# Kernel optimization log

Measured on AMD Instinct MI355X. Metric: run time of the kernel, lower is better.

Reference implementation:

```python
import jax, jax.numpy as jnp
import numpy as np

K_LIST = (1, 5, 20)
IGNORE = -100


def setup_inputs() -> dict:
    key = jax.random.key(0)
    k1, k2 = jax.random.split(key)
    logits = jax.random.normal(k1, (2, 2048, 32000), dtype=jnp.float32)
    labels = jax.random.randint(k2, (2, 2048), 0, 32000, dtype=jnp.int64)
    return {"logits": logits, "labels": labels}


def reference(logits, labels):
    B, S, V = logits.shape
    # shift labels left by one, pad with ignore_index (-100)
    extra = jnp.full((B, 1), IGNORE, dtype=labels.dtype)
    shift_labels = jnp.concatenate([labels[:, 1:], extra], axis=1).reshape(-1)  # [B*S]
    lg = logits.reshape(-1, V)  # [N, V]

    valid = shift_labels >= 0
    safe = jnp.where(valid, shift_labels, 0)
    n_valid = valid.sum().astype(lg.dtype)

    # cross entropy per token (Fast_CrossEntropyLoss equivalent)
    lp = jax.nn.log_softmax(lg, axis=-1)  # [N, V]
    ce = -jnp.take_along_axis(lp, safe[:, None], axis=-1)[:, 0]  # [N]
    ce = jnp.where(valid, ce, 0.0)
    loss = ce.sum() / n_valid  # focal_loss_gamma == 0 -> plain mean over valid

    # categorical entropy per token: -sum p * log p
    entropy = -jnp.sum(jnp.exp(lp) * lp, axis=-1)  # [N]
    entropy = jnp.where(valid, entropy, 0.0)

    # top-k accuracies (k = 1, 5, 20) over valid tokens
    _, topk = jax.lax.top_k(lg, max(K_LIST))  # [N, 20]
    hits = topk == safe[:, None]  # [N, 20]
    accs = tuple(
        (jnp.any(hits[:, :k], axis=-1) & valid).sum().astype(lg.dtype) / n_valid
        for k in K_LIST
    )

    # Note: per-token ce/entropy are returned full-length with zeros at
    # invalid positions (jit-compatible masking instead of boolean gather).
    return (loss, ce, entropy, *accs)
```

## Files before the change

### kernel.cpp

```cpp
#include <hip/hip_runtime.h>
#include <math.h>

#define VOCAB 32000
#define NV4   (VOCAB / 4)
#define BLK   256
#define SEQ   2048
#define IGNORE_IDX (-100)

__device__ inline void merge_state(float& m, float& s, float& t,
                                   float om, float os, float ot) {
    float mm = fmaxf(m, om);
    float ca = __expf(m - mm);
    float cb = __expf(om - mm);
    t = ca * (t + (m - mm) * s) + cb * (ot + (om - mm) * os);
    s = ca * s + cb * os;
    m = mm;
}

__global__ void init_ws_kernel(float* ws) {
    if (threadIdx.x < 8) ws[threadIdx.x] = 0.0f;
}

__global__ __launch_bounds__(BLK)
void ce_metrics_kernel(const float* __restrict__ logits,
                       const int* __restrict__ labels,
                       float* __restrict__ out,
                       float* __restrict__ ws,
                       int N)
{
    const int n = blockIdx.x;
    const int pos = n % SEQ;

    float* ce_out  = out + 1;
    float* ent_out = out + 1 + N;

    int label = (pos < SEQ - 1) ? labels[n + 1] : IGNORE_IDX;

    if (label < 0) {
        if (threadIdx.x == 0) { ce_out[n] = 0.0f; ent_out[n] = 0.0f; }
        return;
    }

    const float* __restrict__ row = logits + (size_t)n * VOCAB;
    const float x_label = row[label];
    const float4* __restrict__ row4 = (const float4*)row;

    float m = -3.402823466e38f;
    float s = 0.0f, t = 0.0f;
    int cgt = 0;
    int ceq = 0;

    for (int i = threadIdx.x; i < NV4; i += BLK) {
        float4 x4 = row4[i];
        const float xs[4] = {x4.x, x4.y, x4.z, x4.w};
        #pragma unroll
        for (int j = 0; j < 4; ++j) {
            float x = xs[j];
            if (x > m) {
                float c = __expf(m - x);
                t = c * (t + (m - x) * s);
                s = c * s + 1.0f;
                m = x;
            } else {
                float d = x - m;
                float e = __expf(d);
                s += e;
                t += e * d;
            }
            cgt += (x > x_label) ? 1 : 0;
            ceq += (x == x_label && (4 * i + j) < label) ? 1 : 0;
        }
    }

    #pragma unroll
    for (int mask = 32; mask > 0; mask >>= 1) {
        float om = __shfl_xor(m, mask);
        float os = __shfl_xor(s, mask);
        float ot = __shfl_xor(t, mask);
        cgt += __shfl_xor(cgt, mask);
        ceq += __shfl_xor(ceq, mask);
        merge_state(m, s, t, om, os, ot);
    }

    __shared__ float sm[4], ss[4], st[4];
    __shared__ int sgt[4], seq_[4];
    const int wid  = threadIdx.x >> 6;
    const int lane = threadIdx.x & 63;
    if (lane == 0) { sm[wid] = m; ss[wid] = s; st[wid] = t; sgt[wid] = cgt; seq_[wid] = ceq; }
    __syncthreads();

    if (threadIdx.x == 0) {
        m = sm[0]; s = ss[0]; t = st[0]; cgt = sgt[0]; ceq = seq_[0];
        #pragma unroll
        for (int w = 1; w < 4; ++w) {
            merge_state(m, s, t, sm[w], ss[w], st[w]);
            cgt += sgt[w];
            ceq += seq_[w];
        }
        float logs = logf(s);
        float ce   = m + logs - x_label;
        float ent  = logs - t / s;
        ce_out[n]  = ce;
        ent_out[n] = ent;

        int rank = cgt + ceq;
        atomicAdd(&ws[0], ce);
        atomicAdd(&ws[1], 1.0f);
        if (rank < 1)  atomicAdd(&ws[2], 1.0f);
        if (rank < 5)  atomicAdd(&ws[3], 1.0f);
        if (rank < 20) atomicAdd(&ws[4], 1.0f);
    }
}

__global__ void finalize_kernel(const float* __restrict__ ws,
                                float* __restrict__ out, int N) {
    if (threadIdx.x == 0) {
        float nv = ws[1];
        out[0]         = ws[0] / nv;
        out[1 + 2 * N]     = ws[2] / nv;
        out[1 + 2 * N + 1] = ws[3] / nv;
        out[1 + 2 * N + 2] = ws[4] / nv;
    }
}

extern "C" void kernel_launch(void* const* d_in, const int* in_sizes, int n_in,
                              void* d_out, int out_size, void* d_ws, size_t ws_size,
                              hipStream_t stream) {
    const float* logits = (const float*)d_in[0];
    const int*   labels = (const int*)d_in[1];
    float* out = (float*)d_out;
    float* ws  = (float*)d_ws;

    const int N = in_sizes[1];

    init_ws_kernel<<<1, 64, 0, stream>>>(ws);
    ce_metrics_kernel<<<N, BLK, 0, stream>>>(logits, labels, out, ws, N);
    finalize_kernel<<<1, 64, 0, stream>>>(ws, out, N);
}
```

Before: 716.5 us.

## Map one wavefront per token, vectorize online softmax, replace atomics with two-pass reduction

Each token row is now handled by one 64-lane wavefront instead of a 256-thread block, which removes the shared-memory and __syncthreads cross-wave merge. The per-element branchy online softmax becomes a branch-free update done once per float4, using the max of four elements and a fixed, unrolled trip count. Global atomics and the init kernel are replaced by a per-token rank written to the workspace and a single-block finalize reduction. In exchange each wave streams a 128KB row alone, so more memory parallelism has to come from occupancy across waves, and the finalize pass adds a serial single-block sweep over N entries.

```diff
diff --git a/kernel.cpp b/kernel.cpp
--- a/kernel.cpp
+++ b/kernel.cpp
@@ -3,77 +3,82 @@
 
 #define VOCAB 32000
 #define NV4   (VOCAB / 4)
-#define BLK   256
 #define SEQ   2048
+#define ITERS (NV4 / 64)
 #define IGNORE_IDX (-100)
 
 __device__ inline void merge_state(float& m, float& s, float& t,
                                    float om, float os, float ot) {
     float mm = fmaxf(m, om);
-    float ca = __expf(m - mm);
-    float cb = __expf(om - mm);
-    t = ca * (t + (m - mm) * s) + cb * (ot + (om - mm) * os);
+    float da = fmaxf(m - mm, -64.0f);
+    float db = fmaxf(om - mm, -64.0f);
+    float ca = __expf(da);
+    float cb = __expf(db);
+    t = ca * (t + da * s) + cb * (ot + db * os);
     s = ca * s + cb * os;
     m = mm;
 }
 
-__global__ void init_ws_kernel(float* ws) {
-    if (threadIdx.x < 8) ws[threadIdx.x] = 0.0f;
-}
-
-__global__ __launch_bounds__(BLK)
+__global__ __launch_bounds__(256)
 void ce_metrics_kernel(const float* __restrict__ logits,
                        const int* __restrict__ labels,
                        float* __restrict__ out,
                        float* __restrict__ ws,
                        int N)
 {
-    const int n = blockIdx.x;
-    const int pos = n % SEQ;
+    const int token = (blockIdx.x << 2) + (threadIdx.x >> 6);
+    const int lane  = threadIdx.x & 63;
+    if (token >= N) return;
 
     float* ce_out  = out + 1;
     float* ent_out = out + 1 + N;
 
-    int label = (pos < SEQ - 1) ? labels[n + 1] : IGNORE_IDX;
+    const int pos = token & (SEQ - 1);
+    const int label = (pos < SEQ - 1) ? labels[token + 1] : IGNORE_IDX;
 
     if (label < 0) {
-        if (threadIdx.x == 0) { ce_out[n] = 0.0f; ent_out[n] = 0.0f; }
+        if (lane == 0) { ce_out[token] = 0.0f; ent_out[token] = 0.0f; ws[token] = -1.0f; }
         return;
     }
 
-    const float* __restrict__ row = logits + (size_t)n * VOCAB;
-    const float x_label = row[label];
+    const float* __restrict__ row = logits + (size_t)token * VOCAB;
+    const float xl = row[label];
     const float4* __restrict__ row4 = (const float4*)row;
 
-    float m = -3.402823466e38f;
-    float s = 0.0f, t = 0.0f;
+    float m = -3.402823466e38f, s = 0.0f, t = 0.0f;
     int cgt = 0;
     int ceq = 0;
 
-    for (int i = threadIdx.x; i < NV4; i += BLK) {
-        float4 x4 = row4[i];
-        const float xs[4] = {x4.x, x4.y, x4.z, x4.w};
-        #pragma unroll
-        for (int j = 0; j < 4; ++j) {
-            float x = xs[j];
-            if (x > m) {
-                float c = __expf(m - x);
-                t = c * (t + (m - x) * s);
-                s = c * s + 1.0f;
-                m = x;
-            } else {
-                float d = x - m;
-                float e = __expf(d);
-                s += e;
-                t += e * d;
-            }
-            cgt += (x > x_label) ? 1 : 0;
-            ceq += (x == x_label && (4 * i + j) < label) ? 1 : 0;
-        }
+    #pragma unroll 5
+    for (int it = 0; it < ITERS; ++it) {
+        const int i4 = it * 64 + lane;
+        float4 x4 = row4[i4];
+
+        float m4 = fmaxf(fmaxf(x4.x, x4.y), fmaxf(x4.z, x4.w));
+        float nm = fmaxf(m, m4);
+        float d1 = fmaxf(m - nm, -64.0f);
+        float c  = __expf(d1);
+        float cs = c * s;
+        t = fmaf(d1, cs, c * t);
+        s = cs;
+        m = nm;
+
+        float dx = x4.x - m, dy = x4.y - m, dz = x4.z - m, dw = x4.w - m;
+        float ex = __expf(dx), ey = __expf(dy), ez = __expf(dz), ew = __expf(dw);
+        s += (ex + ey) + (ez + ew);
+        t = fmaf(ex, dx, t); t = fmaf(ey, dy, t);
+        t = fmaf(ez, dz, t); t = fmaf(ew, dw, t);
+
+        const int base = i4 << 2;
+        cgt += (x4.x > xl) + (x4.y > xl) + (x4.z > xl) + (x4.w > xl);
+        ceq += ((x4.x == xl) & (base     < label))
+             + ((x4.y == xl) & (base + 1 < label))
+             + ((x4.z == xl) & (base + 2 < label))
+             + ((x4.w == xl) & (base + 3 < label));
     }
 
     #pragma unroll
-    for (int mask = 32; mask > 0; mask >>= 1) {
+    for (int mask = 32; mask; mask >>= 1) {
         float om = __shfl_xor(m, mask);
         float os = __shfl_xor(s, mask);
         float ot = __shfl_xor(t, mask);
@@ -82,44 +87,55 @@
         merge_state(m, s, t, om, os, ot);
     }
 
-    __shared__ float sm[4], ss[4], st[4];
-    __shared__ int sgt[4], seq_[4];
-    const int wid  = threadIdx.x >> 6;
-    const int lane = threadIdx.x & 63;
-    if (lane == 0) { sm[wid] = m; ss[wid] = s; st[wid] = t; sgt[wid] = cgt; seq_[wid] = ceq; }
-    __syncthreads();
-
-    if (threadIdx.x == 0) {
-        m = sm[0]; s = ss[0]; t = st[0]; cgt = sgt[0]; ceq = seq_[0];
-        #pragma unroll
-        for (int w = 1; w < 4; ++w) {
-            merge_state(m, s, t, sm[w], ss[w], st[w]);
-            cgt += sgt[w];
-            ceq += seq_[w];
-        }
+    if (lane == 0) {
         float logs = logf(s);
-        float ce   = m + logs - x_label;
-        float ent  = logs - t / s;
-        ce_out[n]  = ce;
-        ent_out[n] = ent;
-
-        int rank = cgt + ceq;
-        atomicAdd(&ws[0], ce);
-        atomicAdd(&ws[1], 1.0f);
-        if (rank < 1)  atomicAdd(&ws[2], 1.0f);
-        if (rank < 5)  atomicAdd(&ws[3], 1.0f);
-        if (rank < 20) atomicAdd(&ws[4], 1.0f);
+        ce_out[token]  = m + logs - xl;
+        ent_out[token] = logs - t / s;
+        ws[token] = (float)(cgt + ceq);
     }
 }
 
-__global__ void finalize_kernel(const float* __restrict__ ws,
-                                float* __restrict__ out, int N) {
+__global__ __launch_bounds__(256)
+void finalize_kernel(const float* __restrict__ ws,
+                     float* __restrict__ out, int N)
+{
+    const float* ce = out + 1;
+    float ce_sum = 0.f, nv = 0.f, h1 = 0.f, h5 = 0.f, h20 = 0.f;
+    for (int i = threadIdx.x; i < N; i += 256) {
+        float r = ws[i];
+        if (r >= 0.f) {
+            nv     += 1.f;
+            ce_sum += ce[i];
+            h1  += (r < 1.f)  ? 1.f : 0.f;
+            h5  += (r < 5.f)  ? 1.f : 0.f;
+            h20 += (r < 20.f) ? 1.f : 0.f;
+        }
+    }
+    #pragma unroll
+    for (int mask = 32; mask; mask >>= 1) {
+        ce_sum += __shfl_xor(ce_sum, mask);
+        nv     += __shfl_xor(nv, mask);
+        h1     += __shfl_xor(h1, mask);
+        h5     += __shfl_xor(h5, mask);
+        h20    += __shfl_xor(h20, mask);
+    }
+    __shared__ float red[5][4];
+    const int wid = threadIdx.x >> 6, lane = threadIdx.x & 63;
+    if (lane == 0) {
+        red[0][wid] = ce_sum; red[1][wid] = nv;
+        red[2][wid] = h1; red[3][wid] = h5; red[4][wid] = h20;
+    }
+    __syncthreads();
     if (threadIdx.x == 0) {
-        float nv = ws[1];
-        out[0]         = ws[0] / nv;
-        out[1 + 2 * N]     = ws[2] / nv;
-        out[1 + 2 * N + 1] = ws[3] / nv;
-        out[1 + 2 * N + 2] = ws[4] / nv;
+        ce_sum = red[0][0] + red[0][1] + red[0][2] + red[0][3];
+        nv     = red[1][0] + red[1][1] + red[1][2] + red[1][3];
+        h1     = red[2][0] + red[2][1] + red[2][2] + red[2][3];
+        h5     = red[3][0] + red[3][1] + red[3][2] + red[3][3];
+        h20    = red[4][0] + red[4][1] + red[4][2] + red[4][3];
+        out[0]         = ce_sum / nv;
+        out[1 + 2*N]     = h1  / nv;
+        out[1 + 2*N + 1] = h5  / nv;
+        out[1 + 2*N + 2] = h20 / nv;
     }
 }
 
@@ -133,7 +149,6 @@
 
     const int N = in_sizes[1];
 
-    init_ws_kernel<<<1, 64, 0, stream>>>(ws);
-    ce_metrics_kernel<<<N, BLK, 0, stream>>>(logits, labels, out, ws, N);
-    finalize_kernel<<<1, 64, 0, stream>>>(ws, out, N);
+    ce_metrics_kernel<<<(N + 3) / 4, 256, 0, stream>>>(logits, labels, out, ws, N);
+    finalize_kernel<<<1, 256, 0, stream>>>(ws, out, N);
 }
```

After: 679.7 us. 5.1% less time.
